# Optimization experiments

Hardware: AMD Instinct MI355X
Metric: run time of the kernel (lower is better)

Reference implementation:

```python
import jax, jax.numpy as jnp
import numpy as np

N, C_IN, C_HID, C_OUT = 50000, 256, 64 * 4, 64
E = 1_600_000
P_DROP = 0.5


def setup_inputs() -> dict:
    key = jax.random.key(0)
    ks = jax.random.split(key, 12)
    cat = C_IN + C_HID  # DConv input is concat([X, H]) -> in+hidden channels
    glorot = lambda k, sh: jax.random.normal(k, sh, jnp.float32) * (2.0 / (sh[-2] + sh[-1])) ** 0.5
    inp = {
        "x": jax.random.normal(ks[0], (N, C_IN), jnp.float32),
        "edge_index": jax.random.randint(ks[1], (2, E), 0, N, jnp.int64),
        "edge_weight": jax.random.uniform(ks[2], (E,), jnp.float32),
        # deterministic dropout mask (training-mode dropout, p=0.5), pre-scaled by 1/(1-p)
        "mask": (jax.random.uniform(ks[3], (N, C_IN)) >= P_DROP).astype(jnp.float32) / (1.0 - P_DROP),
        # DConv weights: shape (2, K=1, in+hidden, hidden) per gate
        "w_z": glorot(ks[4], (2, 1, cat, C_HID)),
        "b_z": jnp.zeros((C_HID,), jnp.float32),
        "w_r": glorot(ks[5], (2, 1, cat, C_HID)),
        "b_r": jnp.zeros((C_HID,), jnp.float32),
        "w_h": glorot(ks[6], (2, 1, cat, C_HID)),
        "b_h": jnp.zeros((C_HID,), jnp.float32),
        "w_lin": glorot(ks[7], (C_OUT, C_HID)),
        "b_lin": jnp.zeros((C_OUT,), jnp.float32),
    }
    return inp


def _dconv(inp, w, b):
    # K=1 diffusion conv: only the zeroth-order (identity) term of both the
    # forward- and backward-transition expansions survives; edges are unused.
    return inp @ w[0, 0] + inp @ w[1, 0] + b


def reference(x, edge_index, edge_weight, mask, w_z, b_z, w_r, b_r, w_h, b_h, w_lin, b_lin):
    x = x * mask  # F.dropout, training=True, deterministic mask
    H = jnp.zeros((x.shape[0], w_z.shape[-1]), x.dtype)  # initial hidden state
    xh = jnp.concatenate([x, H], axis=1)                  # [N, in+hid]
    Z = jax.nn.sigmoid(_dconv(xh, w_z, b_z))              # update gate
    R = jax.nn.sigmoid(_dconv(xh, w_r, b_r))              # reset gate
    xhr = jnp.concatenate([x, H * R], axis=1)
    H_tilde = jnp.tanh(_dconv(xhr, w_h, b_h))             # candidate state
    H = Z * H + (1.0 - Z) * H_tilde                       # GRU blend
    h = jax.nn.elu(H)
    return h @ w_lin.T + b_lin                            # [N, out]
```

## Files before the change

### kernel.cpp

```cpp
#include <hip/hip_runtime.h>
#include <hip/hip_bf16.h>


typedef __attribute__((ext_vector_type(8))) short bf16x8;
typedef __attribute__((ext_vector_type(4))) float f32x4;

constexpr int N_ROWS = 50000;
constexpr int CIN  = 256;
constexpr int COUT = 64;
constexpr int BM   = 64;

__device__ inline unsigned short f2bf(float f) {
    union { float f; unsigned u; } v; v.f = f;
    unsigned r = v.u + 0x7fffu + ((v.u >> 16) & 1u);
    return (unsigned short)(r >> 16);
}
__device__ inline f32x4 mfma16(bf16x8 a, bf16x8 b, f32x4 c) {
    return __builtin_amdgcn_mfma_f32_16x16x32_bf16(a, b, c, 0, 0, 0);
}
__device__ __forceinline__ void gload16(const void* g, void* l) {
    __builtin_amdgcn_global_load_lds(
        (const __attribute__((address_space(1))) char*)g,
        (__attribute__((address_space(3))) char*)l, 16, 0, 0);
}

__global__ __launch_bounds__(256) void prep_frags(
    const float* __restrict__ wz, const float* __restrict__ wh,
    const float* __restrict__ wlin, unsigned short* __restrict__ ws)
{
    int t = blockIdx.x * 256 + threadIdx.x;
    int frag = t >> 6, lane = t & 63;
    if (frag >= 288) return;
    int g16 = lane & 15, kg = lane >> 4;
    unsigned short vals[8];
    if (frag < 256) {
        int kb = frag & 7, nf = (frag >> 3) & 15, g = frag >> 7;
        const float* wsrc = g ? wh : wz;
        int n = nf * 16 + g16;
        #pragma unroll
        for (int j = 0; j < 8; ++j) {
            int k = kb * 32 + kg * 8 + j;
            float v = wsrc[k * 256 + n] + wsrc[131072 + k * 256 + n];
            vals[j] = f2bf(v);
        }
    } else {
        int f = frag - 256;
        int kb = f & 7, nf = f >> 3;
        int n = nf * 16 + g16;
        #pragma unroll
        for (int j = 0; j < 8; ++j) {
            int k = kb * 32 + kg * 8 + j;
            vals[j] = f2bf(wlin[n * 256 + k]);
        }
    }
    unsigned short* dst = ws + (size_t)frag * 512 + lane * 8;
    #pragma unroll
    for (int j = 0; j < 8; ++j) dst[j] = vals[j];
}

__device__ inline bf16x8 ldfrag(const unsigned short* wf, int frag, int lane) {
    return *reinterpret_cast<const bf16x8*>(wf + (size_t)frag * 512 + lane * 8);
}

__global__ __launch_bounds__(512)
__attribute__((amdgpu_waves_per_eu(4, 4)))
void dcrnn_async(
    const float* __restrict__ x, const float* __restrict__ mask,
    const unsigned short* __restrict__ wf,
    const float* __restrict__ bz, const float* __restrict__ bh,
    const float* __restrict__ blin, float* __restrict__ out)
{
    __shared__ char smem[65536];
    char* AhiB = smem;
    const int tid = threadIdx.x, lane = tid & 63, wv = tid >> 6;
    const int l16 = lane & 15, lk = lane >> 4;
    const int row0 = blockIdx.x * BM;
    const int nf0 = wv * 2;
    char* wbuf = smem + 32768 + wv * 4096;

    auto stage_both = [&](int kb) {
        gload16(wf + (size_t)((nf0)          * 8 + kb) * 512 + lane * 8, wbuf);
        gload16(wf + (size_t)((nf0 + 1)      * 8 + kb) * 512 + lane * 8, wbuf + 1024);
        gload16(wf + (size_t)((16 + nf0)     * 8 + kb) * 512 + lane * 8, wbuf + 2048);
        gload16(wf + (size_t)((16 + nf0 + 1) * 8 + kb) * 512 + lane * 8, wbuf + 3072);
    };

    stage_both(0);

    float bzv[2], bhv[2];
    #pragma unroll
    for (int nfi = 0; nfi < 2; ++nfi) {
        int col = wv * 32 + nfi * 16 + l16;
        bzv[nfi] = bz[col]; bhv[nfi] = bh[col];
    }
    const int ocol = (wv & 3) * 16 + l16;
    const float bo = blin[ocol];
    const int mo = wv >> 2;

    #pragma unroll
    for (int it = 0; it < 8; ++it) {
        int s = it * 512 + tid, r = s >> 6, c4 = s & 63;
        int row = row0 + r;
        float4 xv = make_float4(0.f, 0.f, 0.f, 0.f), mv = xv;
        if (row < N_ROWS) {
            xv = reinterpret_cast<const float4*>(x    + (size_t)row * CIN)[c4];
            mv = reinterpret_cast<const float4*>(mask + (size_t)row * CIN)[c4];
        }
        unsigned short h0 = f2bf(xv.x * mv.x), h1 = f2bf(xv.y * mv.y);
        unsigned short h2 = f2bf(xv.z * mv.z), h3 = f2bf(xv.w * mv.w);
        int byte = ((r * CIN + c4 * 4) * 2) ^ ((r & 7) << 4);
        *reinterpret_cast<ushort4*>(AhiB + byte) = make_ushort4(h0, h1, h2, h3);
    }
    __syncthreads();

    f32x4 accZ[2][4], accH[2][4];
    #pragma unroll
    for (int nfi = 0; nfi < 2; ++nfi)
        #pragma unroll
        for (int m = 0; m < 4; ++m) {
            accZ[nfi][m] = (f32x4){0.f, 0.f, 0.f, 0.f};
            accH[nfi][m] = (f32x4){0.f, 0.f, 0.f, 0.f};
        }

    for (int kb = 0; kb < 8; ++kb) {
        bf16x8 ah[4];
        int koff = kb * 32 + lk * 8;
        #pragma unroll
        for (int m = 0; m < 4; ++m) {
            int row = m * 16 + l16;
            int byte = ((row * CIN + koff) * 2) ^ ((row & 7) << 4);
            ah[m] = *reinterpret_cast<const bf16x8*>(AhiB + byte);
        }
        asm volatile("s_waitcnt vmcnt(0)" ::: "memory");
        bf16x8 zb0 = *reinterpret_cast<const bf16x8*>(wbuf + lane * 16);
        bf16x8 zb1 = *reinterpret_cast<const bf16x8*>(wbuf + 1024 + lane * 16);
        bf16x8 hb0 = *reinterpret_cast<const bf16x8*>(wbuf + 2048 + lane * 16);
        bf16x8 hb1 = *reinterpret_cast<const bf16x8*>(wbuf + 3072 + lane * 16);
        asm volatile("s_waitcnt lgkmcnt(0)" ::: "memory");
        if (kb < 7) stage_both(kb + 1);
        #pragma unroll
        for (int m = 0; m < 4; ++m) {
            accZ[0][m] = mfma16(ah[m], zb0, accZ[0][m]);
            accZ[1][m] = mfma16(ah[m], zb1, accZ[1][m]);
        }
        #pragma unroll
        for (int m = 0; m < 4; ++m) {
            accH[0][m] = mfma16(ah[m], hb0, accH[0][m]);
            accH[1][m] = mfma16(ah[m], hb1, accH[1][m]);
        }
    }
    bf16x8 cb = ldfrag(wf, 256 + (wv & 3) * 8, lane);
    __syncthreads();

    #pragma unroll
    for (int nfi = 0; nfi < 2; ++nfi) {
        int col = wv * 32 + nfi * 16 + l16;
        #pragma unroll
        for (int m = 0; m < 4; ++m) {
            #pragma unroll
            for (int i = 0; i < 4; ++i) {
                float z  = 1.f / (1.f + __expf(-(accZ[nfi][m][i] + bzv[nfi])));
                float tt = __expf(2.f * (accH[nfi][m][i] + bhv[nfi]));
                float th = (tt - 1.f) / (tt + 1.f);
                float H  = (1.f - z) * th;
                float h  = (H > 0.f) ? H : (__expf(H) - 1.f);
                int row = m * 16 + lk * 4 + i;
                unsigned pk = ((unsigned)f2bf(h)) << 16;
                int byte = (row * 1024 + col * 4) ^ ((row & 7) << 4);
                *reinterpret_cast<unsigned*>(smem + byte) = pk;
            }
        }
    }
    __syncthreads();

    f32x4 accO[2];
    accO[0] = (f32x4){0.f, 0.f, 0.f, 0.f};
    accO[1] = (f32x4){0.f, 0.f, 0.f, 0.f};
    for (int kb = 0; kb < 8; ++kb) {
        int nk = kb < 7 ? kb + 1 : 7;
        bf16x8 nb = ldfrag(wf, 256 + (wv & 3) * 8 + nk, lane);
        #pragma unroll
        for (int m = 0; m < 2; ++m) {
            int row = mo * 32 + m * 16 + l16;
            int e0  = kb * 32 + lk * 8;
            int b0  = (row * 1024 + e0 * 4)      ^ ((row & 7) << 4);
            int b1  = (row * 1024 + e0 * 4 + 16) ^ ((row & 7) << 4);
            uint4 p0 = *reinterpret_cast<const uint4*>(smem + b0);
            uint4 p1 = *reinterpret_cast<const uint4*>(smem + b1);
            bf16x8 ha;
            ha[0] = (short)(p0.x >> 16); ha[1] = (short)(p0.y >> 16);
            ha[2] = (short)(p0.z >> 16); ha[3] = (short)(p0.w >> 16);
            ha[4] = (short)(p1.x >> 16); ha[5] = (short)(p1.y >> 16);
            ha[6] = (short)(p1.z >> 16); ha[7] = (short)(p1.w >> 16);
            accO[m] = mfma16(ha, cb, accO[m]);
        }
        cb = nb;
    }
    #pragma unroll
    for (int m = 0; m < 2; ++m)
        #pragma unroll
        for (int i = 0; i < 4; ++i) {
            int row = row0 + mo * 32 + m * 16 + lk * 4 + i;
            if (row < N_ROWS) out[(size_t)row * COUT + ocol] = accO[m][i] + bo;
        }
}

__global__ __launch_bounds__(256) void fallback_f32(
    const float* __restrict__ x, const float* __restrict__ mask,
    const float* __restrict__ wzr, const float* __restrict__ whr,
    const float* __restrict__ bz, const float* __restrict__ bh,
    const float* __restrict__ wlinr, const float* __restrict__ blin,
    float* __restrict__ out)
{
    __shared__ float xm[32][CIN];
    const int tid = threadIdx.x;
    const int row0 = blockIdx.x * 32;
    #pragma unroll
    for (int it = 0; it < 8; ++it) {
        int idx = it * 256 + tid;
        int r = idx >> 6, c4 = idx & 63, row = row0 + r;
        float4 v = make_float4(0.f, 0.f, 0.f, 0.f);
        if (row < N_ROWS) {
            float4 a = reinterpret_cast<const float4*>(x    + (size_t)row * CIN)[c4];
            float4 m = reinterpret_cast<const float4*>(mask + (size_t)row * CIN)[c4];
            v = make_float4(a.x * m.x, a.y * m.y, a.z * m.z, a.w * m.w);
        }
        reinterpret_cast<float4*>(&xm[r][0])[c4] = v;
    }
    __syncthreads();
    const int j0 = (tid & 63) * 4, r0 = (tid >> 6) * 8;
    float accz[4][8], acch[4][8];
    #pragma unroll
    for (int c = 0; c < 4; ++c)
        #pragma unroll
        for (int r = 0; r < 8; ++r) { accz[c][r] = 0.f; acch[c][r] = 0.f; }
    for (int k = 0; k < CIN; k += 4) {
        float4 wz4[4], wh4[4];
        #pragma unroll
        for (int kk = 0; kk < 4; ++kk) {
            float4 a0 = *reinterpret_cast<const float4*>(&wzr[(k + kk) * 256 + j0]);
            float4 a1 = *reinterpret_cast<const float4*>(&wzr[131072 + (k + kk) * 256 + j0]);
            wz4[kk] = make_float4(a0.x + a1.x, a0.y + a1.y, a0.z + a1.z, a0.w + a1.w);
            float4 b0 = *reinterpret_cast<const float4*>(&whr[(k + kk) * 256 + j0]);
            float4 b1 = *reinterpret_cast<const float4*>(&whr[131072 + (k + kk) * 256 + j0]);
            wh4[kk] = make_float4(b0.x + b1.x, b0.y + b1.y, b0.z + b1.z, b0.w + b1.w);
        }
        #pragma unroll
        for (int r = 0; r < 8; ++r) {
            float4 xv = *reinterpret_cast<const float4*>(&xm[r0 + r][k]);
            float xk[4] = {xv.x, xv.y, xv.z, xv.w};
            float wzc[4][4] = {{wz4[0].x,wz4[0].y,wz4[0].z,wz4[0].w},{wz4[1].x,wz4[1].y,wz4[1].z,wz4[1].w},
                               {wz4[2].x,wz4[2].y,wz4[2].z,wz4[2].w},{wz4[3].x,wz4[3].y,wz4[3].z,wz4[3].w}};
            float whc[4][4] = {{wh4[0].x,wh4[0].y,wh4[0].z,wh4[0].w},{wh4[1].x,wh4[1].y,wh4[1].z,wh4[1].w},
                               {wh4[2].x,wh4[2].y,wh4[2].z,wh4[2].w},{wh4[3].x,wh4[3].y,wh4[3].z,wh4[3].w}};
            #pragma unroll
            for (int kk = 0; kk < 4; ++kk)
                #pragma unroll
                for (int c = 0; c < 4; ++c) {
                    accz[c][r] = fmaf(xk[kk], wzc[kk][c], accz[c][r]);
                    acch[c][r] = fmaf(xk[kk], whc[kk][c], acch[c][r]);
                }
        }
    }
    float bzj[4], bhj[4];
    #pragma unroll
    for (int c = 0; c < 4; ++c) { bzj[c] = bz[j0 + c]; bhj[c] = bh[j0 + c]; }
    __syncthreads();
    #pragma unroll
    for (int r = 0; r < 8; ++r) {
        float hc[4];
        #pragma unroll
        for (int c = 0; c < 4; ++c) {
            float z  = 1.f / (1.f + expf(-(accz[c][r] + bzj[c])));
            float ht = tanhf(acch[c][r] + bhj[c]);
            float H  = (1.f - z) * ht;
            hc[c] = (H > 0.f) ? H : expm1f(H);
        }
        *reinterpret_cast<float4*>(&xm[r0 + r][j0]) = make_float4(hc[0], hc[1], hc[2], hc[3]);
    }
    __syncthreads();
    const int o = tid & 63;
    float acc[8];
    #pragma unroll
    for (int r = 0; r < 8; ++r) acc[r] = 0.f;
    for (int k = 0; k < CIN; k += 4) {
        float4 wv4 = *reinterpret_cast<const float4*>(&wlinr[o * 256 + k]);
        #pragma unroll
        for (int r = 0; r < 8; ++r) {
            float4 hv = *reinterpret_cast<const float4*>(&xm[r0 + r][k]);
            acc[r] = fmaf(hv.x, wv4.x, acc[r]);
            acc[r] = fmaf(hv.y, wv4.y, acc[r]);
            acc[r] = fmaf(hv.z, wv4.z, acc[r]);
            acc[r] = fmaf(hv.w, wv4.w, acc[r]);
        }
    }
    float bo = blin[o];
    #pragma unroll
    for (int r = 0; r < 8; ++r) {
        int row = row0 + r0 + r;
        if (row < N_ROWS) out[(size_t)row * COUT + o] = acc[r] + bo;
    }
}

extern "C" void kernel_launch(void* const* d_in, const int* in_sizes, int n_in,
                              void* d_out, int out_size, void* d_ws, size_t ws_size,
                              hipStream_t stream)
{
    const float* x    = (const float*)d_in[0];
    const float* mask = (const float*)d_in[3];
    const float* wz   = (const float*)d_in[4];
    const float* bz   = (const float*)d_in[5];
    const float* wh   = (const float*)d_in[8];
    const float* bh   = (const float*)d_in[9];
    const float* wlin = (const float*)d_in[10];
    const float* blin = (const float*)d_in[11];
    float* outf = (float*)d_out;

    const size_t ws_need = 288 * 1024;
    if (ws_size >= ws_need) {
        unsigned short* wsf = (unsigned short*)d_ws;
        prep_frags<<<72, 256, 0, stream>>>(wz, wh, wlin, wsf);
        dcrnn_async<<<(N_ROWS + BM - 1) / BM, 512, 0, stream>>>(
            x, mask, wsf, bz, bh, blin, outf);
    } else {
        fallback_f32<<<(N_ROWS + 31) / 32, 256, 0, stream>>>(
            x, mask, wz, wh, bz, bh, wlin, blin, outf);
    }
}
```

Measured before the change: 61.11 us.

## Overlap second-half activation loads with first gate MFMA iterations

The kernel now stages only the first 128 input channels of x*mask into LDS before starting the gate GEMM. The remaining columns are loaded into registers and written to LDS while k-blocks 0-3 run. The gate loop is fully unrolled, with split per-weight vmcnt waits so the Z and H weight prefetches are issued and waited on separately. The output GEMM now double-buffers its weight fragments two steps ahead. The fine-grained waitcnt constants depend on the exact count of outstanding loads, so a miscount could create a race or stalls, and register pressure rises.

```diff
diff --git a/kernel.cpp b/kernel.cpp
--- a/kernel.cpp
+++ b/kernel.cpp
@@ -61,6 +61,44 @@
 __device__ inline bf16x8 ldfrag(const unsigned short* wf, int frag, int lane) {
     return *reinterpret_cast<const bf16x8*>(wf + (size_t)frag * 512 + lane * 8);
 }
+
+#define GATE_ITER(KB, WZ, WH, SN)                                                   \
+    do {                                                                            \
+        bf16x8 ah[4];                                                               \
+        int koff = (KB) * 32 + lk * 8;                                              \
+        _Pragma("unroll")                                                           \
+        for (int m = 0; m < 4; ++m) {                                               \
+            int row = m * 16 + l16;                                                 \
+            int byte = ((row * CIN + koff) * 2) ^ ((row & 7) << 4);                 \
+            ah[m] = *reinterpret_cast<const bf16x8*>(AhiB + byte);                  \
+        }                                                                           \
+        asm volatile("s_waitcnt vmcnt(" WZ ")" ::: "memory");                       \
+        bf16x8 zb0 = *reinterpret_cast<const bf16x8*>(wbuf + lane * 16);            \
+        bf16x8 zb1 = *reinterpret_cast<const bf16x8*>(wbuf + 1024 + lane * 16);     \
+        asm volatile("s_waitcnt lgkmcnt(0)" ::: "memory");                          \
+        if (SN) {                                                                   \
+            gload16(wf + (size_t)((nf0)     * 8 + (KB) + 1) * 512 + lane * 8, wbuf);\
+            gload16(wf + (size_t)((nf0 + 1) * 8 + (KB) + 1) * 512 + lane * 8, wbuf + 1024);\
+        }                                                                           \
+        _Pragma("unroll")                                                           \
+        for (int m = 0; m < 4; ++m) {                                               \
+            accZ[0][m] = mfma16(ah[m], zb0, accZ[0][m]);                            \
+            accZ[1][m] = mfma16(ah[m], zb1, accZ[1][m]);                            \
+        }                                                                           \
+        asm volatile("s_waitcnt vmcnt(" WH ")" ::: "memory");                       \
+        bf16x8 hb0 = *reinterpret_cast<const bf16x8*>(wbuf + 2048 + lane * 16);     \
+        bf16x8 hb1 = *reinterpret_cast<const bf16x8*>(wbuf + 3072 + lane * 16);     \
+        asm volatile("s_waitcnt lgkmcnt(0)" ::: "memory");                          \
+        if (SN) {                                                                   \
+            gload16(wf + (size_t)((16 + nf0)     * 8 + (KB) + 1) * 512 + lane * 8, wbuf + 2048);\
+            gload16(wf + (size_t)((16 + nf0 + 1) * 8 + (KB) + 1) * 512 + lane * 8, wbuf + 3072);\
+        }                                                                           \
+        _Pragma("unroll")                                                           \
+        for (int m = 0; m < 4; ++m) {                                               \
+            accH[0][m] = mfma16(ah[m], hb0, accH[0][m]);                            \
+            accH[1][m] = mfma16(ah[m], hb1, accH[1][m]);                            \
+        }                                                                           \
+    } while (0)
 
 __global__ __launch_bounds__(512)
 __attribute__((amdgpu_waves_per_eu(4, 4)))
@@ -78,14 +116,10 @@
     const int nf0 = wv * 2;
     char* wbuf = smem + 32768 + wv * 4096;
 
-    auto stage_both = [&](int kb) {
-        gload16(wf + (size_t)((nf0)          * 8 + kb) * 512 + lane * 8, wbuf);
-        gload16(wf + (size_t)((nf0 + 1)      * 8 + kb) * 512 + lane * 8, wbuf + 1024);
-        gload16(wf + (size_t)((16 + nf0)     * 8 + kb) * 512 + lane * 8, wbuf + 2048);
-        gload16(wf + (size_t)((16 + nf0 + 1) * 8 + kb) * 512 + lane * 8, wbuf + 3072);
-    };
-
-    stage_both(0);
+    gload16(wf + (size_t)((nf0)          * 8) * 512 + lane * 8, wbuf);
+    gload16(wf + (size_t)((nf0 + 1)      * 8) * 512 + lane * 8, wbuf + 1024);
+    gload16(wf + (size_t)((16 + nf0)     * 8) * 512 + lane * 8, wbuf + 2048);
+    gload16(wf + (size_t)((16 + nf0 + 1) * 8) * 512 + lane * 8, wbuf + 3072);
 
     float bzv[2], bhv[2];
     #pragma unroll
@@ -97,21 +131,37 @@
     const float bo = blin[ocol];
     const int mo = wv >> 2;
 
-    #pragma unroll
-    for (int it = 0; it < 8; ++it) {
-        int s = it * 512 + tid, r = s >> 6, c4 = s & 63;
+    const int r_st  = (tid >> 5);
+    const int c4_lo = tid & 31;
+    #pragma unroll
+    for (int it = 0; it < 4; ++it) {
+        int r = it * 16 + r_st;
         int row = row0 + r;
         float4 xv = make_float4(0.f, 0.f, 0.f, 0.f), mv = xv;
         if (row < N_ROWS) {
-            xv = reinterpret_cast<const float4*>(x    + (size_t)row * CIN)[c4];
-            mv = reinterpret_cast<const float4*>(mask + (size_t)row * CIN)[c4];
+            xv = reinterpret_cast<const float4*>(x    + (size_t)row * CIN)[c4_lo];
+            mv = reinterpret_cast<const float4*>(mask + (size_t)row * CIN)[c4_lo];
         }
         unsigned short h0 = f2bf(xv.x * mv.x), h1 = f2bf(xv.y * mv.y);
         unsigned short h2 = f2bf(xv.z * mv.z), h3 = f2bf(xv.w * mv.w);
-        int byte = ((r * CIN + c4 * 4) * 2) ^ ((r & 7) << 4);
+        int byte = ((r * CIN + c4_lo * 4) * 2) ^ ((r & 7) << 4);
         *reinterpret_cast<ushort4*>(AhiB + byte) = make_ushort4(h0, h1, h2, h3);
     }
     __syncthreads();
+
+    const int c4_hi = 32 + (tid & 31);
+    float4 px[2], pm[2];
+    #pragma unroll
+    for (int j = 0; j < 2; ++j) {
+        int r = j * 16 + r_st;
+        int row = row0 + r;
+        px[j] = make_float4(0.f, 0.f, 0.f, 0.f); pm[j] = px[j];
+        if (row < N_ROWS) {
+            px[j] = reinterpret_cast<const float4*>(x    + (size_t)row * CIN)[c4_hi];
+            pm[j] = reinterpret_cast<const float4*>(mask + (size_t)row * CIN)[c4_hi];
+        }
+    }
+    __builtin_amdgcn_sched_barrier(0);
 
     f32x4 accZ[2][4], accH[2][4];
     #pragma unroll
@@ -122,34 +172,49 @@
             accH[nfi][m] = (f32x4){0.f, 0.f, 0.f, 0.f};
         }
 
-    for (int kb = 0; kb < 8; ++kb) {
-        bf16x8 ah[4];
-        int koff = kb * 32 + lk * 8;
-        #pragma unroll
-        for (int m = 0; m < 4; ++m) {
-            int row = m * 16 + l16;
-            int byte = ((row * CIN + koff) * 2) ^ ((row & 7) << 4);
-            ah[m] = *reinterpret_cast<const bf16x8*>(AhiB + byte);
-        }
-        asm volatile("s_waitcnt vmcnt(0)" ::: "memory");
-        bf16x8 zb0 = *reinterpret_cast<const bf16x8*>(wbuf + lane * 16);
-        bf16x8 zb1 = *reinterpret_cast<const bf16x8*>(wbuf + 1024 + lane * 16);
-        bf16x8 hb0 = *reinterpret_cast<const bf16x8*>(wbuf + 2048 + lane * 16);
-        bf16x8 hb1 = *reinterpret_cast<const bf16x8*>(wbuf + 3072 + lane * 16);
-        asm volatile("s_waitcnt lgkmcnt(0)" ::: "memory");
-        if (kb < 7) stage_both(kb + 1);
-        #pragma unroll
-        for (int m = 0; m < 4; ++m) {
-            accZ[0][m] = mfma16(ah[m], zb0, accZ[0][m]);
-            accZ[1][m] = mfma16(ah[m], zb1, accZ[1][m]);
-        }
-        #pragma unroll
-        for (int m = 0; m < 4; ++m) {
-            accH[0][m] = mfma16(ah[m], hb0, accH[0][m]);
-            accH[1][m] = mfma16(ah[m], hb1, accH[1][m]);
-        }
-    }
-    bf16x8 cb = ldfrag(wf, 256 + (wv & 3) * 8, lane);
+    GATE_ITER(0, "63", "63", 1);
+    GATE_ITER(1, "2", "2", 1);
+
+    #pragma unroll
+    for (int j = 0; j < 2; ++j) {
+        int r = j * 16 + r_st;
+        unsigned short h0 = f2bf(px[j].x * pm[j].x), h1 = f2bf(px[j].y * pm[j].y);
+        unsigned short h2 = f2bf(px[j].z * pm[j].z), h3 = f2bf(px[j].w * pm[j].w);
+        int byte = ((r * CIN + c4_hi * 4) * 2) ^ ((r & 7) << 4);
+        *reinterpret_cast<ushort4*>(AhiB + byte) = make_ushort4(h0, h1, h2, h3);
+    }
+    #pragma unroll
+    for (int j = 0; j < 2; ++j) {
+        int r = (2 + j) * 16 + r_st;
+        int row = row0 + r;
+        px[j] = make_float4(0.f, 0.f, 0.f, 0.f); pm[j] = px[j];
+        if (row < N_ROWS) {
+            px[j] = reinterpret_cast<const float4*>(x    + (size_t)row * CIN)[c4_hi];
+            pm[j] = reinterpret_cast<const float4*>(mask + (size_t)row * CIN)[c4_hi];
+        }
+    }
+    __builtin_amdgcn_sched_barrier(0);
+
+    GATE_ITER(2, "6", "6", 1);
+
+    #pragma unroll
+    for (int j = 0; j < 2; ++j) {
+        int r = (2 + j) * 16 + r_st;
+        unsigned short h0 = f2bf(px[j].x * pm[j].x), h1 = f2bf(px[j].y * pm[j].y);
+        unsigned short h2 = f2bf(px[j].z * pm[j].z), h3 = f2bf(px[j].w * pm[j].w);
+        int byte = ((r * CIN + c4_hi * 4) * 2) ^ ((r & 7) << 4);
+        *reinterpret_cast<ushort4*>(AhiB + byte) = make_ushort4(h0, h1, h2, h3);
+    }
+
+    GATE_ITER(3, "2", "2", 1);
+    __syncthreads();
+    GATE_ITER(4, "63", "63", 1);
+    GATE_ITER(5, "2", "2", 1);
+    GATE_ITER(6, "2", "2", 1);
+    GATE_ITER(7, "2", "0", 0);
+
+    bf16x8 cb0 = ldfrag(wf, 256 + (wv & 3) * 8 + 0, lane);
+    bf16x8 cb1 = ldfrag(wf, 256 + (wv & 3) * 8 + 1, lane);
     __syncthreads();
 
     #pragma unroll
@@ -176,9 +241,13 @@
     f32x4 accO[2];
     accO[0] = (f32x4){0.f, 0.f, 0.f, 0.f};
     accO[1] = (f32x4){0.f, 0.f, 0.f, 0.f};
+    #pragma unroll
     for (int kb = 0; kb < 8; ++kb) {
-        int nk = kb < 7 ? kb + 1 : 7;
-        bf16x8 nb = ldfrag(wf, 256 + (wv & 3) * 8 + nk, lane);
+        bf16x8 cur = (kb & 1) ? cb1 : cb0;
+        if (kb + 2 < 8) {
+            bf16x8 nf_ = ldfrag(wf, 256 + (wv & 3) * 8 + kb + 2, lane);
+            if (kb & 1) cb1 = nf_; else cb0 = nf_;
+        }
         #pragma unroll
         for (int m = 0; m < 2; ++m) {
             int row = mo * 32 + m * 16 + l16;
@@ -192,9 +261,8 @@
             ha[2] = (short)(p0.z >> 16); ha[3] = (short)(p0.w >> 16);
             ha[4] = (short)(p1.x >> 16); ha[5] = (short)(p1.y >> 16);
             ha[6] = (short)(p1.z >> 16); ha[7] = (short)(p1.w >> 16);
-            accO[m] = mfma16(ha, cb, accO[m]);
-        }
-        cb = nb;
+            accO[m] = mfma16(ha, cur, accO[m]);
+        }
     }
     #pragma unroll
     for (int m = 0; m < 2; ++m)
```

New measurement: 76.99 us. +26.0%, slower.
